# Performance work log

Measured on AMD Instinct MI355X. Metric: run time of the kernel, lower is better.

## Reference

```python
import jax, jax.numpy as jnp
import numpy as np


def setup_inputs() -> dict:
    key = jax.random.key(0)
    x = jax.random.normal(key, (8192, 8192), dtype=jnp.float32)
    return {"x": x, "k": 64}


def reference(x, k):
    # k-th largest value per row: equivalent to sort-descending[..., k-1],
    # but computed with an O(n) partial selection instead of a full sort.
    topv = jax.lax.top_k(x, k)[0]          # [B, k]
    kth = topv[..., -1:]                   # [B, 1] k-th largest
    return x * (x >= kth).astype(x.dtype)  # keep values >= k-th largest
```

## Files before the change

### kernel.cpp

```cpp
#include <hip/hip_runtime.h>
#include <stdint.h>

#define NT 512
#define ROW 8192
#define VPT 4

__device__ __forceinline__ uint32_t f2u(uint32_t b) {
    return (b & 0x80000000u) ? ~b : (b | 0x80000000u);
}
__device__ __forceinline__ uint32_t u2fbits(uint32_t u) {
    return (u & 0x80000000u) ? (u ^ 0x80000000u) : ~u;
}

template <int B>
__device__ __forceinline__ void select_digit(const uint32_t* s_hist, uint32_t* s_wsum,
                                             uint32_t* s_sel, int t, uint32_t k) {
    uint32_t local = 0;
    if (B == 8) {
        uint4 h0 = ((const uint4*)s_hist)[t * 2];
        uint4 h1 = ((const uint4*)s_hist)[t * 2 + 1];
        local = h0.x + h0.y + h0.z + h0.w + h1.x + h1.y + h1.z + h1.w;
    } else {
        uint2 h = ((const uint2*)s_hist)[t];
        local = h.x + h.y;
    }
    const int lane = t & 63;
    const int wave = t >> 6;
    uint32_t incl = local;
#pragma unroll
    for (int off = 1; off < 64; off <<= 1) {
        uint32_t vv = __shfl_down(incl, off, 64);
        if (lane + off < 64) incl += vv;
    }
    if (lane == 0) s_wsum[wave] = incl;
    __syncthreads();
    uint32_t later = 0;
#pragma unroll
    for (int w = 0; w < 8; ++w)
        if (w > wave) later += s_wsum[w];
    const uint32_t sfx_incl = incl + later;
    const uint32_t sfx_excl = sfx_incl - local;
    if (sfx_excl < k && k <= sfx_incl) {
        uint32_t cum = sfx_excl;
#pragma unroll
        for (int i = B - 1; i >= 0; --i) {
            uint32_t c = s_hist[t * B + i];
            if (k <= cum + c) {
                s_sel[0] = (uint32_t)(t * B + i);
                s_sel[1] = k - cum;
                break;
            }
            cum += c;
        }
    }
    __syncthreads();
}

__global__ __launch_bounds__(NT, 8) void ksparse_rowtopk(const float* __restrict__ x,
                                                         const int* __restrict__ kp,
                                                         float* __restrict__ out) {
    __shared__ uint32_t s_hist1[4096];
    __shared__ uint32_t s_hist2[1024];
    __shared__ uint32_t s_wsum[8];
    __shared__ uint32_t s_sel[2];

    const int t = threadIdx.x;
    const long long rowbase = (long long)blockIdx.x * (long long)ROW;
    const uint4* xin = (const uint4*)(x + rowbase);

    uint4 v[VPT];
#pragma unroll
    for (int j = 0; j < VPT; ++j) v[j] = xin[j * NT + t];

    ((uint4*)s_hist1)[t] = make_uint4(0u, 0u, 0u, 0u);
    ((uint4*)s_hist1)[t + NT] = make_uint4(0u, 0u, 0u, 0u);
    if (t < 256) ((uint4*)s_hist2)[t] = make_uint4(0u, 0u, 0u, 0u);

    int kin = *kp;
    if (kin < 1) kin = 1;
    if (kin > ROW) kin = ROW;
    uint32_t k = (uint32_t)kin;
    __syncthreads();

#pragma unroll
    for (int j = 0; j < VPT; ++j) {
        v[j].x = f2u(v[j].x);
        v[j].y = f2u(v[j].y);
        v[j].z = f2u(v[j].z);
        v[j].w = f2u(v[j].w);
        atomicAdd(&s_hist1[v[j].x >> 20], 1u);
        atomicAdd(&s_hist1[v[j].y >> 20], 1u);
        atomicAdd(&s_hist1[v[j].z >> 20], 1u);
        atomicAdd(&s_hist1[v[j].w >> 20], 1u);
    }
    __syncthreads();
    select_digit<8>(s_hist1, s_wsum, s_sel, t, k);
    const uint32_t d1 = s_sel[0];
    k = s_sel[1];

    if (t < 256) ((uint4*)s_hist1)[t] = make_uint4(0u, 0u, 0u, 0u);
#pragma unroll
    for (int j = 0; j < VPT; ++j) {
        if ((v[j].x >> 20) == d1) atomicAdd(&s_hist2[(v[j].x >> 10) & 1023u], 1u);
        if ((v[j].y >> 20) == d1) atomicAdd(&s_hist2[(v[j].y >> 10) & 1023u], 1u);
        if ((v[j].z >> 20) == d1) atomicAdd(&s_hist2[(v[j].z >> 10) & 1023u], 1u);
        if ((v[j].w >> 20) == d1) atomicAdd(&s_hist2[(v[j].w >> 10) & 1023u], 1u);
    }
    __syncthreads();
    select_digit<2>(s_hist2, s_wsum, s_sel, t, k);
    const uint32_t d2 = s_sel[0];
    k = s_sel[1];

    const uint32_t pfx2 = (d1 << 10) | d2;
#pragma unroll
    for (int j = 0; j < VPT; ++j) {
        if ((v[j].x >> 10) == pfx2) atomicAdd(&s_hist1[v[j].x & 1023u], 1u);
        if ((v[j].y >> 10) == pfx2) atomicAdd(&s_hist1[v[j].y & 1023u], 1u);
        if ((v[j].z >> 10) == pfx2) atomicAdd(&s_hist1[v[j].z & 1023u], 1u);
        if ((v[j].w >> 10) == pfx2) atomicAdd(&s_hist1[v[j].w & 1023u], 1u);
    }
    __syncthreads();
    select_digit<2>(s_hist1, s_wsum, s_sel, t, k);
    const uint32_t d3 = s_sel[0];

    const uint32_t thr = (d1 << 20) | (d2 << 10) | d3;

    float4* orow = (float4*)(out + rowbase);
#pragma unroll
    for (int j = 0; j < VPT; ++j) {
        float4 o;
        o.x = (v[j].x >= thr) ? __uint_as_float(u2fbits(v[j].x)) : 0.0f;
        o.y = (v[j].y >= thr) ? __uint_as_float(u2fbits(v[j].y)) : 0.0f;
        o.z = (v[j].z >= thr) ? __uint_as_float(u2fbits(v[j].z)) : 0.0f;
        o.w = (v[j].w >= thr) ? __uint_as_float(u2fbits(v[j].w)) : 0.0f;
        orow[j * NT + t] = o;
    }
}

extern "C" void kernel_launch(void* const* d_in, const int* in_sizes, int n_in,
                              void* d_out, int out_size, void* d_ws, size_t ws_size,
                              hipStream_t stream) {
    const float* x = (const float*)d_in[0];
    const int* kp = (const int*)d_in[1];
    float* out = (float*)d_out;
    const int rows = in_sizes[0] / ROW;
    ksparse_rowtopk<<<dim3(rows), dim3(NT), 0, stream>>>(x, kp, out);
}
```

Baseline: 435.2 us.

## Process multiple rows per block with register double-buffered prefetch

Each block now loops over eight rows and prefetches the next row into a second register buffer while running the radix-select histograms on the current row. Loads and stores use nontemporal builtins to avoid cache pollution. This aims to hide global memory latency behind the shared-memory histogram and sync phases and to cut block launch overhead. In exchange it doubles register use, lowers the occupancy target, and shrinks the grid to one eighth, which can reduce the parallelism available across CUs.

```diff
diff --git a/kernel.cpp b/kernel.cpp
--- a/kernel.cpp
+++ b/kernel.cpp
@@ -4,6 +4,10 @@
 #define NT 512
 #define ROW 8192
 #define VPT 4
+#define RPB 8
+
+typedef unsigned int u32x4 __attribute__((ext_vector_type(4)));
+typedef float f32x4 __attribute__((ext_vector_type(4)));
 
 __device__ __forceinline__ uint32_t f2u(uint32_t b) {
     return (b & 0x80000000u) ? ~b : (b | 0x80000000u);
@@ -56,84 +60,104 @@
     __syncthreads();
 }
 
-__global__ __launch_bounds__(NT, 8) void ksparse_rowtopk(const float* __restrict__ x,
+__global__ __launch_bounds__(NT, 4) void ksparse_rowtopk(const float* __restrict__ x,
                                                          const int* __restrict__ kp,
-                                                         float* __restrict__ out) {
+                                                         float* __restrict__ out,
+                                                         int nrows) {
     __shared__ uint32_t s_hist1[4096];
     __shared__ uint32_t s_hist2[1024];
     __shared__ uint32_t s_wsum[8];
     __shared__ uint32_t s_sel[2];
 
     const int t = threadIdx.x;
-    const long long rowbase = (long long)blockIdx.x * (long long)ROW;
-    const uint4* xin = (const uint4*)(x + rowbase);
-
-    uint4 v[VPT];
-#pragma unroll
-    for (int j = 0; j < VPT; ++j) v[j] = xin[j * NT + t];
-
-    ((uint4*)s_hist1)[t] = make_uint4(0u, 0u, 0u, 0u);
-    ((uint4*)s_hist1)[t + NT] = make_uint4(0u, 0u, 0u, 0u);
-    if (t < 256) ((uint4*)s_hist2)[t] = make_uint4(0u, 0u, 0u, 0u);
+    const long long row0 = (long long)blockIdx.x * RPB;
 
     int kin = *kp;
     if (kin < 1) kin = 1;
     if (kin > ROW) kin = ROW;
-    uint32_t k = (uint32_t)kin;
-    __syncthreads();
+    const uint32_t k0 = (uint32_t)kin;
+
+    u32x4 A[VPT], B[VPT];
+    if (row0 < nrows) {
+        const u32x4* xin = (const u32x4*)(x + row0 * ROW);
+#pragma unroll
+        for (int j = 0; j < VPT; ++j) A[j] = __builtin_nontemporal_load(&xin[j * NT + t]);
+    }
 
 #pragma unroll
-    for (int j = 0; j < VPT; ++j) {
-        v[j].x = f2u(v[j].x);
-        v[j].y = f2u(v[j].y);
-        v[j].z = f2u(v[j].z);
-        v[j].w = f2u(v[j].w);
-        atomicAdd(&s_hist1[v[j].x >> 20], 1u);
-        atomicAdd(&s_hist1[v[j].y >> 20], 1u);
-        atomicAdd(&s_hist1[v[j].z >> 20], 1u);
-        atomicAdd(&s_hist1[v[j].w >> 20], 1u);
-    }
-    __syncthreads();
-    select_digit<8>(s_hist1, s_wsum, s_sel, t, k);
-    const uint32_t d1 = s_sel[0];
-    k = s_sel[1];
+    for (int r = 0; r < RPB; ++r) {
+        const long long row = row0 + r;
+        if (r + 1 < RPB && row + 1 < nrows) {
+            const u32x4* xn = (const u32x4*)(x + (row + 1) * ROW);
+#pragma unroll
+            for (int j = 0; j < VPT; ++j) B[j] = __builtin_nontemporal_load(&xn[j * NT + t]);
+        }
+        if (row < nrows) {
+            ((uint4*)s_hist1)[t] = make_uint4(0u, 0u, 0u, 0u);
+            ((uint4*)s_hist1)[t + NT] = make_uint4(0u, 0u, 0u, 0u);
+            if (t < 256) ((uint4*)s_hist2)[t] = make_uint4(0u, 0u, 0u, 0u);
+            __syncthreads();
 
-    if (t < 256) ((uint4*)s_hist1)[t] = make_uint4(0u, 0u, 0u, 0u);
+            uint32_t k = k0;
+
 #pragma unroll
-    for (int j = 0; j < VPT; ++j) {
-        if ((v[j].x >> 20) == d1) atomicAdd(&s_hist2[(v[j].x >> 10) & 1023u], 1u);
-        if ((v[j].y >> 20) == d1) atomicAdd(&s_hist2[(v[j].y >> 10) & 1023u], 1u);
-        if ((v[j].z >> 20) == d1) atomicAdd(&s_hist2[(v[j].z >> 10) & 1023u], 1u);
-        if ((v[j].w >> 20) == d1) atomicAdd(&s_hist2[(v[j].w >> 10) & 1023u], 1u);
-    }
-    __syncthreads();
-    select_digit<2>(s_hist2, s_wsum, s_sel, t, k);
-    const uint32_t d2 = s_sel[0];
-    k = s_sel[1];
+            for (int j = 0; j < VPT; ++j) {
+                A[j].x = f2u(A[j].x);
+                A[j].y = f2u(A[j].y);
+                A[j].z = f2u(A[j].z);
+                A[j].w = f2u(A[j].w);
+                atomicAdd(&s_hist1[A[j].x >> 20], 1u);
+                atomicAdd(&s_hist1[A[j].y >> 20], 1u);
+                atomicAdd(&s_hist1[A[j].z >> 20], 1u);
+                atomicAdd(&s_hist1[A[j].w >> 20], 1u);
+            }
+            __syncthreads();
+            select_digit<8>(s_hist1, s_wsum, s_sel, t, k);
+            const uint32_t d1 = s_sel[0];
+            k = s_sel[1];
 
-    const uint32_t pfx2 = (d1 << 10) | d2;
+            if (t < 256) ((uint4*)s_hist1)[t] = make_uint4(0u, 0u, 0u, 0u);
 #pragma unroll
-    for (int j = 0; j < VPT; ++j) {
-        if ((v[j].x >> 10) == pfx2) atomicAdd(&s_hist1[v[j].x & 1023u], 1u);
-        if ((v[j].y >> 10) == pfx2) atomicAdd(&s_hist1[v[j].y & 1023u], 1u);
-        if ((v[j].z >> 10) == pfx2) atomicAdd(&s_hist1[v[j].z & 1023u], 1u);
-        if ((v[j].w >> 10) == pfx2) atomicAdd(&s_hist1[v[j].w & 1023u], 1u);
-    }
-    __syncthreads();
-    select_digit<2>(s_hist1, s_wsum, s_sel, t, k);
-    const uint32_t d3 = s_sel[0];
+            for (int j = 0; j < VPT; ++j) {
+                if ((A[j].x >> 20) == d1) atomicAdd(&s_hist2[(A[j].x >> 10) & 1023u], 1u);
+                if ((A[j].y >> 20) == d1) atomicAdd(&s_hist2[(A[j].y >> 10) & 1023u], 1u);
+                if ((A[j].z >> 20) == d1) atomicAdd(&s_hist2[(A[j].z >> 10) & 1023u], 1u);
+                if ((A[j].w >> 20) == d1) atomicAdd(&s_hist2[(A[j].w >> 10) & 1023u], 1u);
+            }
+            __syncthreads();
+            select_digit<2>(s_hist2, s_wsum, s_sel, t, k);
+            const uint32_t d2 = s_sel[0];
+            k = s_sel[1];
 
-    const uint32_t thr = (d1 << 20) | (d2 << 10) | d3;
+            const uint32_t pfx2 = (d1 << 10) | d2;
+#pragma unroll
+            for (int j = 0; j < VPT; ++j) {
+                if ((A[j].x >> 10) == pfx2) atomicAdd(&s_hist1[A[j].x & 1023u], 1u);
+                if ((A[j].y >> 10) == pfx2) atomicAdd(&s_hist1[A[j].y & 1023u], 1u);
+                if ((A[j].z >> 10) == pfx2) atomicAdd(&s_hist1[A[j].z & 1023u], 1u);
+                if ((A[j].w >> 10) == pfx2) atomicAdd(&s_hist1[A[j].w & 1023u], 1u);
+            }
+            __syncthreads();
+            select_digit<2>(s_hist1, s_wsum, s_sel, t, k);
+            const uint32_t d3 = s_sel[0];
 
-    float4* orow = (float4*)(out + rowbase);
+            const uint32_t thr = (d1 << 20) | (d2 << 10) | d3;
+
+            f32x4* orow = (f32x4*)(out + row * ROW);
 #pragma unroll
-    for (int j = 0; j < VPT; ++j) {
-        float4 o;
-        o.x = (v[j].x >= thr) ? __uint_as_float(u2fbits(v[j].x)) : 0.0f;
-        o.y = (v[j].y >= thr) ? __uint_as_float(u2fbits(v[j].y)) : 0.0f;
-        o.z = (v[j].z >= thr) ? __uint_as_float(u2fbits(v[j].z)) : 0.0f;
-        o.w = (v[j].w >= thr) ? __uint_as_float(u2fbits(v[j].w)) : 0.0f;
-        orow[j * NT + t] = o;
+            for (int j = 0; j < VPT; ++j) {
+                f32x4 o;
+                o.x = (A[j].x >= thr) ? __uint_as_float(u2fbits(A[j].x)) : 0.0f;
+                o.y = (A[j].y >= thr) ? __uint_as_float(u2fbits(A[j].y)) : 0.0f;
+                o.z = (A[j].z >= thr) ? __uint_as_float(u2fbits(A[j].z)) : 0.0f;
+                o.w = (A[j].w >= thr) ? __uint_as_float(u2fbits(A[j].w)) : 0.0f;
+                __builtin_nontemporal_store(o, &orow[j * NT + t]);
+            }
+        }
+        if (r + 1 < RPB) {
+#pragma unroll
+            for (int j = 0; j < VPT; ++j) A[j] = B[j];
+        }
     }
 }
 
@@ -144,5 +168,6 @@
     const int* kp = (const int*)d_in[1];
     float* out = (float*)d_out;
     const int rows = in_sizes[0] / ROW;
-    ksparse_rowtopk<<<dim3(rows), dim3(NT), 0, stream>>>(x, kp, out);
+    const int grid = (rows + RPB - 1) / RPB;
+    ksparse_rowtopk<<<dim3(grid), dim3(NT), 0, stream>>>(x, kp, out, rows);
 }
```

After: 435.9 us. No clear change (+0.2%).

## Process each row within a single wave using 8-bit radix passes

Applied to the files above, without the earlier changes.

Each row is now handled by one 64-lane wave that holds all 8192 values in registers, instead of by a 512-thread block. The wave uses a private LDS histogram with four replicated bins to reduce atomic contention. Selection becomes four 8-bit radix passes that use only wave-level shuffles and ballots, with no block-wide barriers. Each wave loops over four rows, and loads and stores are nontemporal. The aim is to remove __syncthreads costs and cross-wave reductions, at the cost of heavy register use (128 values per lane), lower occupancy, a smaller grid of 256 blocks, and one extra histogram pass.

```diff
diff --git a/kernel.cpp b/kernel.cpp
--- a/kernel.cpp
+++ b/kernel.cpp
@@ -2,8 +2,15 @@
 #include <stdint.h>
 
 #define NT 512
+#define NWAVE 8
 #define ROW 8192
-#define VPT 4
+#define QPL 32
+#define RPW 4
+#define NBIN 256
+#define REP 4
+
+typedef unsigned int u32x4 __attribute__((ext_vector_type(4)));
+typedef float f32x4 __attribute__((ext_vector_type(4)));
 
 __device__ __forceinline__ uint32_t f2u(uint32_t b) {
     return (b & 0x80000000u) ? ~b : (b | 0x80000000u);
@@ -11,129 +18,144 @@
 __device__ __forceinline__ uint32_t u2fbits(uint32_t u) {
     return (u & 0x80000000u) ? (u ^ 0x80000000u) : ~u;
 }
+__device__ __forceinline__ void lds_fence() {
+    asm volatile("s_waitcnt lgkmcnt(0)" ::: "memory");
+}
 
-template <int B>
-__device__ __forceinline__ void select_digit(const uint32_t* s_hist, uint32_t* s_wsum,
-                                             uint32_t* s_sel, int t, uint32_t k) {
-    uint32_t local = 0;
-    if (B == 8) {
-        uint4 h0 = ((const uint4*)s_hist)[t * 2];
-        uint4 h1 = ((const uint4*)s_hist)[t * 2 + 1];
-        local = h0.x + h0.y + h0.z + h0.w + h1.x + h1.y + h1.z + h1.w;
-    } else {
-        uint2 h = ((const uint2*)s_hist)[t];
-        local = h.x + h.y;
+__device__ __forceinline__ void hist_clear(uint32_t* hist, int lane) {
+    u32x4 z = {0u, 0u, 0u, 0u};
+#pragma unroll
+    for (int i = 0; i < (NBIN * REP / 4) / 64; ++i)
+        ((u32x4*)hist)[i * 64 + lane] = z;
+}
+
+__device__ __forceinline__ uint32_t wave_select(const uint32_t* hist, int lane,
+                                                uint32_t& k_io) {
+    u32x4 h[4];
+#pragma unroll
+    for (int i = 0; i < 4; ++i) h[i] = ((const u32x4*)hist)[lane * 4 + i];
+    uint32_t b[4], local = 0;
+#pragma unroll
+    for (int i = 0; i < 4; ++i) {
+        b[i] = h[i].x + h[i].y + h[i].z + h[i].w;
+        local += b[i];
     }
-    const int lane = t & 63;
-    const int wave = t >> 6;
     uint32_t incl = local;
 #pragma unroll
     for (int off = 1; off < 64; off <<= 1) {
         uint32_t vv = __shfl_down(incl, off, 64);
         if (lane + off < 64) incl += vv;
     }
-    if (lane == 0) s_wsum[wave] = incl;
-    __syncthreads();
-    uint32_t later = 0;
+    const uint32_t k = k_io;
+    const uint32_t sfx_excl = incl - local;
+    const bool found = (sfx_excl < k) && (k <= incl);
+    uint32_t dig = 0, kn = 0;
+    if (found) {
+        uint32_t cum = sfx_excl;
+        bool done = false;
 #pragma unroll
-    for (int w = 0; w < 8; ++w)
-        if (w > wave) later += s_wsum[w];
-    const uint32_t sfx_incl = incl + later;
-    const uint32_t sfx_excl = sfx_incl - local;
-    if (sfx_excl < k && k <= sfx_incl) {
-        uint32_t cum = sfx_excl;
-#pragma unroll
-        for (int i = B - 1; i >= 0; --i) {
-            uint32_t c = s_hist[t * B + i];
-            if (k <= cum + c) {
-                s_sel[0] = (uint32_t)(t * B + i);
-                s_sel[1] = k - cum;
-                break;
+        for (int i = 3; i >= 0; --i) {
+            if (!done) {
+                if (k <= cum + b[i]) {
+                    dig = (uint32_t)(lane * 4 + i);
+                    kn = k - cum;
+                    done = true;
+                } else {
+                    cum += b[i];
+                }
             }
-            cum += c;
         }
     }
-    __syncthreads();
+    unsigned long long mb = __ballot(found);
+    int src = (int)__ffsll(mb) - 1;
+    dig = (uint32_t)__shfl((int)dig, src, 64);
+    kn = (uint32_t)__shfl((int)kn, src, 64);
+    k_io = kn;
+    return dig;
 }
 
-__global__ __launch_bounds__(NT, 8) void ksparse_rowtopk(const float* __restrict__ x,
+__global__ __launch_bounds__(NT, 2) void ksparse_rowtopk(const float* __restrict__ x,
                                                          const int* __restrict__ kp,
-                                                         float* __restrict__ out) {
-    __shared__ uint32_t s_hist1[4096];
-    __shared__ uint32_t s_hist2[1024];
-    __shared__ uint32_t s_wsum[8];
-    __shared__ uint32_t s_sel[2];
+                                                         float* __restrict__ out,
+                                                         int nrows) {
+    __shared__ uint32_t s_hist[NWAVE][NBIN * REP];
 
-    const int t = threadIdx.x;
-    const long long rowbase = (long long)blockIdx.x * (long long)ROW;
-    const uint4* xin = (const uint4*)(x + rowbase);
-
-    uint4 v[VPT];
-#pragma unroll
-    for (int j = 0; j < VPT; ++j) v[j] = xin[j * NT + t];
-
-    ((uint4*)s_hist1)[t] = make_uint4(0u, 0u, 0u, 0u);
-    ((uint4*)s_hist1)[t + NT] = make_uint4(0u, 0u, 0u, 0u);
-    if (t < 256) ((uint4*)s_hist2)[t] = make_uint4(0u, 0u, 0u, 0u);
+    const int lane = threadIdx.x & 63;
+    const int wv = threadIdx.x >> 6;
+    uint32_t* hist = s_hist[wv];
+    const int rsel = lane & 3;
+    const long long gw = (long long)blockIdx.x * NWAVE + wv;
 
     int kin = *kp;
     if (kin < 1) kin = 1;
     if (kin > ROW) kin = ROW;
-    uint32_t k = (uint32_t)kin;
-    __syncthreads();
+    const uint32_t k0 = (uint32_t)kin;
 
+#pragma unroll 1
+    for (int rr = 0; rr < RPW; ++rr) {
+        const long long row = gw * RPW + rr;
+        if (row >= nrows) break;
+
+        const u32x4* xin = (const u32x4*)(x + row * ROW);
+        u32x4 v[QPL];
 #pragma unroll
-    for (int j = 0; j < VPT; ++j) {
-        v[j].x = f2u(v[j].x);
-        v[j].y = f2u(v[j].y);
-        v[j].z = f2u(v[j].z);
-        v[j].w = f2u(v[j].w);
-        atomicAdd(&s_hist1[v[j].x >> 20], 1u);
-        atomicAdd(&s_hist1[v[j].y >> 20], 1u);
-        atomicAdd(&s_hist1[v[j].z >> 20], 1u);
-        atomicAdd(&s_hist1[v[j].w >> 20], 1u);
-    }
-    __syncthreads();
-    select_digit<8>(s_hist1, s_wsum, s_sel, t, k);
-    const uint32_t d1 = s_sel[0];
-    k = s_sel[1];
+        for (int j = 0; j < QPL; ++j)
+            v[j] = __builtin_nontemporal_load(&xin[j * 64 + lane]);
+#pragma unroll
+        for (int j = 0; j < QPL; ++j) {
+            v[j].x = f2u(v[j].x);
+            v[j].y = f2u(v[j].y);
+            v[j].z = f2u(v[j].z);
+            v[j].w = f2u(v[j].w);
+        }
 
-    if (t < 256) ((uint4*)s_hist1)[t] = make_uint4(0u, 0u, 0u, 0u);
+        uint32_t k = k0;
+
+        hist_clear(hist, lane);
+        lds_fence();
 #pragma unroll
-    for (int j = 0; j < VPT; ++j) {
-        if ((v[j].x >> 20) == d1) atomicAdd(&s_hist2[(v[j].x >> 10) & 1023u], 1u);
-        if ((v[j].y >> 20) == d1) atomicAdd(&s_hist2[(v[j].y >> 10) & 1023u], 1u);
-        if ((v[j].z >> 20) == d1) atomicAdd(&s_hist2[(v[j].z >> 10) & 1023u], 1u);
-        if ((v[j].w >> 20) == d1) atomicAdd(&s_hist2[(v[j].w >> 10) & 1023u], 1u);
-    }
-    __syncthreads();
-    select_digit<2>(s_hist2, s_wsum, s_sel, t, k);
-    const uint32_t d2 = s_sel[0];
-    k = s_sel[1];
+        for (int j = 0; j < QPL; ++j) {
+            atomicAdd(&hist[(v[j].x >> 24) * REP + rsel], 1u);
+            atomicAdd(&hist[(v[j].y >> 24) * REP + rsel], 1u);
+            atomicAdd(&hist[(v[j].z >> 24) * REP + rsel], 1u);
+            atomicAdd(&hist[(v[j].w >> 24) * REP + rsel], 1u);
+        }
+        lds_fence();
+        uint32_t pfx = wave_select(hist, lane, k);
 
-    const uint32_t pfx2 = (d1 << 10) | d2;
+#pragma unroll 1
+        for (int p = 0; p < 3; ++p) {
+            hist_clear(hist, lane);
+            lds_fence();
+            const int mshift = 24 - p * 8;
+            const int bshift = 16 - p * 8;
 #pragma unroll
-    for (int j = 0; j < VPT; ++j) {
-        if ((v[j].x >> 10) == pfx2) atomicAdd(&s_hist1[v[j].x & 1023u], 1u);
-        if ((v[j].y >> 10) == pfx2) atomicAdd(&s_hist1[v[j].y & 1023u], 1u);
-        if ((v[j].z >> 10) == pfx2) atomicAdd(&s_hist1[v[j].z & 1023u], 1u);
-        if ((v[j].w >> 10) == pfx2) atomicAdd(&s_hist1[v[j].w & 1023u], 1u);
-    }
-    __syncthreads();
-    select_digit<2>(s_hist1, s_wsum, s_sel, t, k);
-    const uint32_t d3 = s_sel[0];
+            for (int j = 0; j < QPL; ++j) {
+                if ((v[j].x >> mshift) == pfx)
+                    atomicAdd(&hist[((v[j].x >> bshift) & 255u) * REP + rsel], 1u);
+                if ((v[j].y >> mshift) == pfx)
+                    atomicAdd(&hist[((v[j].y >> bshift) & 255u) * REP + rsel], 1u);
+                if ((v[j].z >> mshift) == pfx)
+                    atomicAdd(&hist[((v[j].z >> bshift) & 255u) * REP + rsel], 1u);
+                if ((v[j].w >> mshift) == pfx)
+                    atomicAdd(&hist[((v[j].w >> bshift) & 255u) * REP + rsel], 1u);
+            }
+            lds_fence();
+            const uint32_t d = wave_select(hist, lane, k);
+            pfx = (pfx << 8) | d;
+        }
+        const uint32_t thr = pfx;
 
-    const uint32_t thr = (d1 << 20) | (d2 << 10) | d3;
-
-    float4* orow = (float4*)(out + rowbase);
+        f32x4* orow = (f32x4*)(out + row * ROW);
 #pragma unroll
-    for (int j = 0; j < VPT; ++j) {
-        float4 o;
-        o.x = (v[j].x >= thr) ? __uint_as_float(u2fbits(v[j].x)) : 0.0f;
-        o.y = (v[j].y >= thr) ? __uint_as_float(u2fbits(v[j].y)) : 0.0f;
-        o.z = (v[j].z >= thr) ? __uint_as_float(u2fbits(v[j].z)) : 0.0f;
-        o.w = (v[j].w >= thr) ? __uint_as_float(u2fbits(v[j].w)) : 0.0f;
-        orow[j * NT + t] = o;
+        for (int j = 0; j < QPL; ++j) {
+            f32x4 o;
+            o.x = (v[j].x >= thr) ? __uint_as_float(u2fbits(v[j].x)) : 0.0f;
+            o.y = (v[j].y >= thr) ? __uint_as_float(u2fbits(v[j].y)) : 0.0f;
+            o.z = (v[j].z >= thr) ? __uint_as_float(u2fbits(v[j].z)) : 0.0f;
+            o.w = (v[j].w >= thr) ? __uint_as_float(u2fbits(v[j].w)) : 0.0f;
+            __builtin_nontemporal_store(o, &orow[j * 64 + lane]);
+        }
     }
 }
 
@@ -144,5 +166,6 @@
     const int* kp = (const int*)d_in[1];
     float* out = (float*)d_out;
     const int rows = in_sizes[0] / ROW;
-    ksparse_rowtopk<<<dim3(rows), dim3(NT), 0, stream>>>(x, kp, out);
+    const int grid = (rows + NWAVE * RPW - 1) / (NWAVE * RPW);
+    ksparse_rowtopk<<<dim3(grid), dim3(NT), 0, stream>>>(x, kp, out, rows);
 }
```

New measurement: 476.9 us. 9.6% more time.
